# Kernel tuning notes

Hardware: AMD Instinct MI355X
Metric: run time of the kernel (lower is better)

## Reference

```python
import jax, jax.numpy as jnp
import numpy as np

N_DIMS = 64
D1 = N_DIMS - 1          # 63, feature dim of xs and of per-head q/k/v in non-last layers
N_EMBD = 2 * N_DIMS      # 128, forced by H + attn residual
N_LAYER = 12
N_HEAD = 4
POINTS = 512
BS = 16
LN_EPS = 1e-5


def setup_inputs() -> dict:
    key = jax.random.key(0)
    ks = jax.random.split(key, 16)
    s = 0.05
    f32 = jnp.float32
    inp = {
        "xs": jax.random.normal(ks[0], (BS, POINTS, D1), f32),
        "ys": jax.random.normal(ks[1], (BS, POINTS), f32),
        "head_mask": jnp.ones((1, N_HEAD, 1, 1), f32),
        # _read_in
        "read_in_W": jax.random.normal(ks[2], (N_DIMS, N_EMBD), f32) * s,
        "read_in_b": jnp.zeros((N_EMBD,), f32),
        # layers 0..n_layer-2: q/v Linear(D1 -> n_head*D1), key linear is unused (identity repeat)
        "qW": jax.random.normal(ks[3], (N_LAYER - 1, D1, N_HEAD * D1), f32) * s,
        "vW": jax.random.normal(ks[4], (N_LAYER - 1, D1, N_HEAD * D1), f32) * s,
        # last layer: q/k/v Linear(n_embd -> n_head*n_embd)
        "qW_last": jax.random.normal(ks[5], (N_EMBD, N_HEAD * N_EMBD), f32) * s,
        "kW_last": jax.random.normal(ks[6], (N_EMBD, N_HEAD * N_EMBD), f32) * s,
        "vW_last": jax.random.normal(ks[7], (N_EMBD, N_HEAD * N_EMBD), f32) * s,
        # layernorms
        "ln1_g": jnp.ones((N_LAYER, N_EMBD), f32),
        "ln1_b": jnp.zeros((N_LAYER, N_EMBD), f32),
        "ln2_g": jnp.ones((N_LAYER, N_EMBD), f32),
        "ln2_b": jnp.zeros((N_LAYER, N_EMBD), f32),
        # MLPs (n_embd -> 4*n_embd -> n_embd)
        "mlp_W1": jax.random.normal(ks[8], (N_LAYER, N_EMBD, 4 * N_EMBD), f32) * s,
        "mlp_b1": jnp.zeros((N_LAYER, 4 * N_EMBD), f32),
        "mlp_W2": jax.random.normal(ks[9], (N_LAYER, 4 * N_EMBD, N_EMBD), f32) * s,
        "mlp_b2": jnp.zeros((N_LAYER, N_EMBD), f32),
        # _read_out
        "read_out_W": jax.random.normal(ks[10], (N_EMBD, 1), f32) * s,
        "read_out_b": jnp.zeros((1,), f32),
    }
    return inp


def _layernorm(x, g, b):
    mu = jnp.mean(x, axis=-1, keepdims=True)
    var = jnp.var(x, axis=-1, keepdims=True)
    return (x - mu) * jax.lax.rsqrt(var + LN_EPS) * g + b


def _forward(xs, ys, head_mask, read_in_W, read_in_b, qW, vW,
             qW_last, kW_last, vW_last, ln1_g, ln1_b, ln2_g, ln2_b,
             mlp_W1, mlp_b1, mlp_W2, mlp_b2, read_out_W, read_out_b):
    bs, P, d = xs.shape  # d = n_dims - 1
    # _combine: interleave x (zero-padded) and (x, y) rows -> [bs, 2P, n_dims]
    xs_e = jnp.concatenate([xs, jnp.zeros((bs, P, 1), xs.dtype)], axis=2)
    ys_w = jnp.concatenate([xs, ys[:, :, None]], axis=2)
    zs = jnp.stack([xs_e, ys_w], axis=2).reshape(bs, 2 * P, d + 1)
    N = 2 * P

    # triangular count-normalization: row i (0-based) has 1/(i+1) on cols <= i
    i = jnp.arange(N)
    maskNorm = jnp.where(i[None, :] <= i[:, None], 1.0 / (i[:, None] + 1.0), 0.0).astype(xs.dtype)

    H = zs @ read_in_W + read_in_b  # [bs, N, n_embd]

    for idx in range(N_LAYER):
        if idx != N_LAYER - 1:
            # q from the "label half" of H, k is identity on the "feature half", v learned
            q = (H[:, :, N_DIMS:2 * N_DIMS - 1] @ qW[idx]).reshape(bs, N, N_HEAD, D1).transpose(0, 2, 1, 3)
            k = jnp.broadcast_to(H[:, None, :, :D1], (bs, N_HEAD, N, D1))
            v = (H[:, :, :D1] @ vW[idx]).reshape(bs, N, N_HEAD, D1).transpose(0, 2, 1, 3)
            # cat((z1[n_dims zeros], ., z2[1 zero])) -> head dim 2*n_dims == n_embd
            pad = ((0, 0), (0, 0), (0, 0), (N_DIMS, 1))
            q = jnp.pad(q, pad) * head_mask
            k = jnp.pad(k, pad) * head_mask
            v = jnp.pad(v, pad) * head_mask
        else:
            q = (H @ qW_last).reshape(bs, N, N_HEAD, N_EMBD).transpose(0, 2, 1, 3) * head_mask
            k = (H @ kW_last).reshape(bs, N, N_HEAD, N_EMBD).transpose(0, 2, 1, 3) * head_mask
            v = (H @ vW_last).reshape(bs, N, N_HEAD, N_EMBD).transpose(0, 2, 1, 3) * head_mask
        scores = jax.nn.relu(jnp.einsum('bhid,bhjd->bhij', q, k)) * maskNorm  # [bs,h,N,N]
        attn = jnp.einsum('bhij,bhjd->bhid', scores, v).sum(axis=1)           # [bs,N,n_embd]
        H = _layernorm(H + attn, ln1_g[idx], ln1_b[idx])
        mlp = jax.nn.relu(H @ mlp_W1[idx] + mlp_b1[idx]) @ mlp_W2[idx] + mlp_b2[idx]
        H = _layernorm(H + mlp, ln2_g[idx], ln2_b[idx])

    pred = H @ read_out_W + read_out_b  # [bs, N, 1]
    return pred[:, ::2, 0]              # [bs, P]


def reference(xs, ys, head_mask, read_in_W, read_in_b, qW, vW,
              qW_last, kW_last, vW_last, ln1_g, ln1_b, ln2_g, ln2_b,
              mlp_W1, mlp_b1, mlp_W2, mlp_b2, read_out_W, read_out_b):
    return _forward(xs, ys, head_mask, read_in_W, read_in_b, qW, vW,
                    qW_last, kW_last, vW_last, ln1_g, ln1_b, ln2_g, ln2_b,
                    mlp_W1, mlp_b1, mlp_W2, mlp_b2, read_out_W, read_out_b)
```

## Files before the change

### kernel.cpp

```cpp
#include <hip/hip_runtime.h>

#define BS 16
#define SEQ 1024
#define EMB 128
#define NHEAD 4
#define LN_EPS 1e-5f

typedef __attribute__((ext_vector_type(8))) short bf16x8;
typedef __attribute__((ext_vector_type(8))) _Float16 f16x8;
typedef __attribute__((ext_vector_type(4))) float f32x4;
typedef __attribute__((ext_vector_type(4))) unsigned short u16x4;
typedef __attribute__((ext_vector_type(4))) unsigned int u32x4;

__device__ __forceinline__ unsigned short f2b(float f) {
  union { float f; unsigned u; } v; v.f = f;
  unsigned r = v.u + 0x7fff + ((v.u >> 16) & 1);
  return (unsigned short)(r >> 16);
}
__device__ __forceinline__ float b2f(unsigned short u) {
  return __uint_as_float((unsigned)u << 16);
}
__device__ __forceinline__ unsigned short f2h(float f) {
  union { _Float16 h; unsigned short u; } v; v.h = (_Float16)f; return v.u;
}
__device__ __forceinline__ void split2(float x, unsigned short& hi, unsigned short& lo) {
  unsigned short h = f2b(x);
  float hf = __uint_as_float((unsigned)h << 16);
  hi = h; lo = f2b(x - hf);
}
__device__ __forceinline__ float rsqrt_acc(float v) {
  float r = rsqrtf(v);
  return r * (1.5f - 0.5f * v * r * r);
}

__global__ void k_prep_fragT(const float* __restrict__ in, unsigned short* __restrict__ out,
                             size_t PL, int L, int Kin, int Nin, int N, int K) {
  int idx = blockIdx.x * 256 + threadIdx.x;
  int nblk = (N >> 4) * (K >> 5);
  int total = L * N * K;
  if (idx >= total) return;
  int e = idx & 7;
  int lane = (idx >> 3) & 63;
  int blk = (idx >> 9) % nblk;
  int l = idx / (512 * nblk);
  int nb = blk % (N >> 4), kc = blk / (N >> 4);
  int n = nb * 16 + (lane & 15);
  int k = kc * 32 + (lane >> 4) * 8 + e;
  float v = (k < Kin && n < Nin) ? in[(size_t)l * Kin * Nin + (size_t)k * Nin + n] : 0.f;
  unsigned short hi, lo; split2(v, hi, lo);
  out[idx] = hi; out[PL + idx] = lo;
}

__global__ void k_prep_qvfrag(const float* __restrict__ qW, const float* __restrict__ vW,
                              unsigned short* __restrict__ out, size_t PL) {
  int idx = blockIdx.x * 256 + threadIdx.x;
  int total = 11 * 512 * 128;
  if (idx >= total) return;
  int e = idx & 7;
  int lane = (idx >> 3) & 63;
  int blk = (idx >> 9) & 127;
  int l = idx >> 16;
  int nb = blk & 31, kc = blk >> 5;
  int n = nb * 16 + (lane & 15);
  int k = kc * 32 + (lane >> 4) * 8 + e;
  float v = 0.f;
  if (n < 256) {
    int hh = n >> 6, d = n & 63;
    if (d < 63 && k >= 64 && k < 127) v = qW[(size_t)l * 63 * 252 + (size_t)(k - 64) * 252 + hh * 63 + d];
  } else {
    int n2 = n - 256, hh = n2 >> 6, d = n2 & 63;
    if (d < 63 && k < 63) v = vW[(size_t)l * 63 * 252 + (size_t)k * 252 + hh * 63 + d];
  }
  unsigned short hi, lo; split2(v, hi, lo);
  out[idx] = hi; out[PL + idx] = lo;
}

__global__ void k_prep_lastfrag(const float* __restrict__ qW, const float* __restrict__ kW,
                                const float* __restrict__ vW,
                                unsigned short* __restrict__ out, size_t PL) {
  int idx = blockIdx.x * 256 + threadIdx.x;
  int total = 1536 * 128;
  if (idx >= total) return;
  int e = idx & 7;
  int lane = (idx >> 3) & 63;
  int blk = idx >> 9;
  int nb = blk % 96, kc = blk / 96;
  int n = nb * 16 + (lane & 15);
  int k = kc * 32 + (lane >> 4) * 8 + e;
  int tsel = n >> 9, n2 = n & 511;
  const float* W = tsel == 0 ? qW : (tsel == 1 ? kW : vW);
  float v = W[(size_t)k * 512 + n2];
  unsigned short hi, lo; split2(v, hi, lo);
  out[idx] = hi; out[PL + idx] = lo;
}

__global__ void k_combine_readin(const float* __restrict__ xs, const float* __restrict__ ys,
                                 const float* __restrict__ W, const float* __restrict__ bias,
                                 unsigned short* __restrict__ Hbf, size_t hbPl,
                                 unsigned short* __restrict__ Hh) {
  int blk = blockIdx.x;
  int b = blk >> 10, t = blk & 1023, p = t >> 1;
  __shared__ float zs[64];
  int tid = threadIdx.x;
  if (tid < 64) {
    float v;
    if (tid < 63) v = xs[((size_t)b * 512 + p) * 63 + tid];
    else v = (t & 1) ? ys[(size_t)b * 512 + p] : 0.f;
    zs[tid] = v;
  }
  __syncthreads();
  float acc = bias[tid];
  #pragma unroll 8
  for (int d = 0; d < 64; ++d) acc += zs[d] * W[d * 128 + tid];
  size_t o = (size_t)blk * 128 + tid;
  unsigned short hi, lo; split2(acc, hi, lo);
  Hbf[o] = hi; Hbf[hbPl + o] = lo;
  if (tid < 64) Hh[(size_t)blk * 64 + tid] = f2h(acc);
}

template<int MODE, bool RELU>
__global__ __launch_bounds__(256) void k_gemm(
    const unsigned short* __restrict__ A, size_t aPl,
    const unsigned short* __restrict__ BT, size_t bPl, const float* __restrict__ bias,
    int N,
    unsigned short* __restrict__ out0,
    unsigned short* __restrict__ out1,
    unsigned short* __restrict__ out2) {
  extern __shared__ unsigned short lds[];
  int tid = threadIdx.x;
  int wid = tid >> 6, lane = tid & 63;
  int lr = lane & 15, lg = lane >> 4;
  int row0g = blockIdx.x * 64;
  int n0 = blockIdx.y * 64;
  unsigned short* Ah = lds;
  unsigned short* Al = Ah + 64 * 136;
  {
    const unsigned short* gA = A + (size_t)row0g * 128;
    const unsigned short* srcs[2] = { gA, gA + aPl };
    unsigned short* dsts[2] = { Ah, Al };
    #pragma unroll
    for (int p = 0; p < 2; ++p)
      #pragma unroll
      for (int it = 0; it < 4; ++it) {
        int e = it * 2048 + tid * 8;
        bf16x8 v = *reinterpret_cast<const bf16x8*>(srcs[p] + e);
        *reinterpret_cast<bf16x8*>(dsts[p] + (e >> 7) * 136 + (e & 127)) = v;
      }
  }
  __syncthreads();
  bf16x8 afh[4], afl[4];
  #pragma unroll
  for (int kf = 0; kf < 4; ++kf) {
    int o = (wid * 16 + lr) * 136 + kf * 32 + lg * 8;
    afh[kf] = *reinterpret_cast<const bf16x8*>(Ah + o);
    afl[kf] = *reinterpret_cast<const bf16x8*>(Al + o);
  }
  f32x4 acc[4] = {};
  int nhw = N >> 4;
  #pragma unroll
  for (int nf = 0; nf < 4; ++nf) {
    #pragma unroll
    for (int kf = 0; kf < 4; ++kf) {
      size_t bo = ((size_t)kf * nhw + (n0 >> 4) + nf) * 512 + lane * 8;
      bf16x8 bh = *reinterpret_cast<const bf16x8*>(BT + bo);
      bf16x8 bl = *reinterpret_cast<const bf16x8*>(BT + bPl + bo);
      acc[nf] = __builtin_amdgcn_mfma_f32_16x16x32_bf16(afh[kf], bh, acc[nf], 0, 0, 0);
      acc[nf] = __builtin_amdgcn_mfma_f32_16x16x32_bf16(afl[kf], bh, acc[nf], 0, 0, 0);
      acc[nf] = __builtin_amdgcn_mfma_f32_16x16x32_bf16(afh[kf], bl, acc[nf], 0, 0, 0);
    }
  }
  __syncthreads();
  #pragma unroll
  for (int nf = 0; nf < 4; ++nf) {
    int c = n0 + nf * 16 + lr;
    float bv = bias ? bias[c] : 0.f;
    #pragma unroll
    for (int r = 0; r < 4; ++r) {
      float v = acc[nf][r] + bv;
      if (RELU) v = fmaxf(v, 0.f);
      int rL = wid * 16 + lg * 4 + r, cL = nf * 16 + lr;
      ((unsigned short(*)[66])lds)[rL][cL] = f2h(v);
    }
  }
  __syncthreads();
  int u = tid * 2;
  int lane2 = u >> 3, e0 = u & 7;
  if (MODE == 2) {
    unsigned short (*t16)[66] = (unsigned short(*)[66])lds;
    int b = row0g >> 10, t0 = row0g & 1023;
    int tsel = n0 >> 9, c2b = n0 & 511, hh = c2b >> 7, dbase = c2b & 127;
    size_t bh = (size_t)b * NHEAD + hh;
    if (tsel < 2) {
      unsigned short* base = tsel ? out1 : out0;
      int tb0 = t0 >> 4, kc0 = dbase >> 5;
      #pragma unroll
      for (int fb = 0; fb < 8; ++fb) {
        int tbl = fb >> 1, kcl = fb & 1;
        int t_l = tbl * 16 + (lane2 & 15);
        int c_l = kcl * 32 + ((lane2 >> 4) << 3) + e0;
        size_t dst = ((bh * 64 + tb0 + tbl) * 4 + kc0 + kcl) * 512 + lane2 * 8 + e0;
        base[dst] = t16[t_l][c_l];
        base[dst + 1] = t16[t_l][c_l + 1];
      }
    } else {
      int db0 = dbase >> 4, jc0 = t0 >> 5;
      #pragma unroll
      for (int fb = 0; fb < 8; ++fb) {
        int dbl = fb >> 1, jcl = fb & 1;
        int c_l = dbl * 16 + (lane2 & 15);
        int t_l = jcl * 32 + ((lane2 >> 4) << 3) + e0;
        size_t dst = ((bh * 8 + db0 + dbl) * 32 + jc0 + jcl) * 512 + lane2 * 8 + e0;
        out2[dst] = t16[t_l][c_l];
        out2[dst + 1] = t16[t_l + 1][c_l];
      }
    }
  } else {
    unsigned short (*t16)[66] = (unsigned short(*)[66])lds;
    int b = row0g >> 10, t0 = row0g & 1023;
    if (n0 < 256) {
      size_t bh = (size_t)b * NHEAD + (n0 >> 6);
      int tb0 = t0 >> 4;
      #pragma unroll
      for (int fb = 0; fb < 8; ++fb) {
        int tbl = fb >> 1, kcl = fb & 1;
        int t_l = tbl * 16 + (lane2 & 15);
        int c_l = kcl * 32 + ((lane2 >> 4) << 3) + e0;
        size_t dst = ((bh * 64 + tb0 + tbl) * 2 + kcl) * 512 + lane2 * 8 + e0;
        out0[dst] = t16[t_l][c_l];
        out0[dst + 1] = t16[t_l][c_l + 1];
      }
    } else {
      size_t bh = (size_t)b * NHEAD + ((n0 - 256) >> 6);
      int jc0 = t0 >> 5;
      #pragma unroll
      for (int fb = 0; fb < 8; ++fb) {
        int dbl = fb >> 1, jcl = fb & 1;
        int c_l = dbl * 16 + (lane2 & 15);
        int t_l = jcl * 32 + ((lane2 >> 4) << 3) + e0;
        size_t dst = ((bh * 4 + dbl) * 32 + jc0 + jcl) * 512 + lane2 * 8 + e0;
        out1[dst] = t16[t_l][c_l];
        out1[dst + 1] = t16[t_l + 1][c_l];
      }
    }
  }
}

__global__ __launch_bounds__(512) void k_attn_v7(
    const unsigned short* __restrict__ q,
    const unsigned short* __restrict__ Hh,
    const unsigned short* __restrict__ vT,
    const float* __restrict__ head_mask,
    const unsigned short* __restrict__ HbfIn, unsigned short* __restrict__ HbfOut, size_t hbPl,
    const float* __restrict__ g, const float* __restrict__ bta) {
  extern __shared__ char sh[];
  int bid = blockIdx.x;
  int xcd = bid & 7, u = bid >> 3;
  int b = xcd * 2 + (u >> 4);
  int pidx = u & 15;
  int tid = threadIdx.x;
  int wid = tid >> 6, lane = tid & 63;
  int h = wid & 3, grp = wid >> 2;
  int lr = lane & 15, lg = lane >> 4;
  int i0t[2] = { pidx * 32, (31 - pidx) * 32 };
  int NSS = (33 - pidx) >> 1;

  const char* gK = (const char*)(Hh + (size_t)b * SEQ * 64);
  char* KB = sh;
  unsigned short* sw = (unsigned short*)(sh + 16384 + wid * 2560);

  const unsigned short* qh = q + (size_t)(b * NHEAD + h) * 65536;
  const unsigned short* vh = vT + (size_t)(b * NHEAD + h) * 65536;

  f16x8 qf[2][2][2];
  #pragma unroll
  for (int t = 0; t < 2; ++t)
    #pragma unroll
    for (int mf = 0; mf < 2; ++mf)
      #pragma unroll
      for (int kf = 0; kf < 2; ++kf)
        qf[t][mf][kf] = *reinterpret_cast<const f16x8*>(
            qh + ((((i0t[t] >> 4) + mf) * 2 + kf) << 9) + lane * 8);
  f32x4 oacc[2][2][4] = {};

  u32x4 sreg;
  auto SLOAD = [&](int ss) {
    sreg = *reinterpret_cast<const u32x4*>(gK + (size_t)ss * 8192 + tid * 16);
  };
  auto SWRITE = [&](int buf) {
    int row = tid >> 3, colb = (tid & 7) * 16;
    *reinterpret_cast<u32x4*>(KB + buf * 8192 + row * 128 + (colb ^ ((row & 7) << 4))) = sreg;
  };

  SLOAD(0); SWRITE(0);
  __syncthreads();

  for (int ss = 0; ss < NSS; ++ss) {
    int cur = ss & 1;
    bool more = (ss + 1 < NSS);
    if (more) SLOAD(ss + 1);
    int js = ss * 64 + grp * 32;
    if (js < i0t[1] + 32) {
      f16x8 vch[4];
      #pragma unroll
      for (int nf = 0; nf < 4; ++nf)
        vch[nf] = *reinterpret_cast<const f16x8*>(vh + ((nf * 32 + (js >> 5)) << 9) + lane * 8);
      f16x8 kfr[2][2];
      #pragma unroll
      for (int nf2 = 0; nf2 < 2; ++nf2)
        #pragma unroll
        for (int kf = 0; kf < 2; ++kf) {
          int row = grp * 32 + nf2 * 16 + lr;
          int colb = kf * 64 + lg * 16;
          kfr[nf2][kf] = *reinterpret_cast<const f16x8*>(
              KB + cur * 8192 + row * 128 + (colb ^ ((row & 7) << 4)));
        }
      #pragma unroll
      for (int t = 0; t < 2; ++t) {
        if (js < i0t[t] + 32) {
          #pragma unroll
          for (int nf2 = 0; nf2 < 2; ++nf2) {
            #pragma unroll
            for (int mf = 0; mf < 2; ++mf) {
              f32x4 sacc = {};
              #pragma unroll
              for (int kf = 0; kf < 2; ++kf)
                sacc = __builtin_amdgcn_mfma_f32_16x16x32_f16(qf[t][mf][kf], kfr[nf2][kf], sacc, 0, 0, 0);
              #pragma unroll
              for (int r = 0; r < 4; ++r) {
                int i = i0t[t] + mf * 16 + lg * 4 + r;
                int j = js + nf2 * 16 + lr;
                float v = (j <= i) ? fmaxf(sacc[r], 0.f) : 0.f;
                sw[(mf * 16 + lg * 4 + r) * 40 + nf2 * 16 + lr] = f2h(v);
              }
            }
          }
          asm volatile("s_waitcnt lgkmcnt(0)" ::: "memory");
          __builtin_amdgcn_sched_barrier(0);
          #pragma unroll
          for (int mf = 0; mf < 2; ++mf) {
            f16x8 sf = *reinterpret_cast<const f16x8*>(&sw[(mf * 16 + lr) * 40 + lg * 8]);
            #pragma unroll
            for (int nf = 0; nf < 4; ++nf)
              oacc[t][mf][nf] = __builtin_amdgcn_mfma_f32_16x16x32_f16(sf, vch[nf], oacc[t][mf][nf], 0, 0, 0);
          }
        }
      }
    }
    if (more) SWRITE(cur ^ 1);
    __syncthreads();
  }

  float hm = head_mask[h];
  float hm3 = hm * hm * hm;
  float* f8 = (float*)sh;
  for (int t = 0; t < 2; ++t) {
    #pragma unroll
    for (int mf = 0; mf < 2; ++mf)
      #pragma unroll
      for (int nf = 0; nf < 4; ++nf)
        #pragma unroll
        for (int r = 0; r < 4; ++r)
          f8[wid * 2048 + (mf * 16 + lg * 4 + r) * 64 + nf * 16 + lr] = oacc[t][mf][nf][r] * hm3;
    __syncthreads();
    for (int idx = tid; idx < 8192; idx += 512) f8[idx] += f8[idx + 8192];
    __syncthreads();
    for (int idx = tid; idx < 4096; idx += 512) f8[idx] += f8[idx + 4096];
    __syncthreads();
    for (int idx = tid; idx < 2048; idx += 512) {
      int rr = idx >> 6;
      f8[idx] = (f8[idx] + f8[idx + 2048]) / (float)(i0t[t] + rr + 1);
    }
    __syncthreads();
    for (int rl = 0; rl < 4; ++rl) {
      int rr = wid * 4 + rl;
      size_t row = ((size_t)b * SEQ + i0t[t] + rr) * EMB;
      int c0 = lane, c1 = lane + 64;
      float x0 = b2f(HbfIn[row + c0]) + b2f(HbfIn[hbPl + row + c0]);
      float x1 = b2f(HbfIn[row + c1]) + b2f(HbfIn[hbPl + row + c1]) + f8[rr * 64 + lane];
      float s1 = x0 + x1, s2 = x0 * x0 + x1 * x1;
      #pragma unroll
      for (int off = 1; off < 64; off <<= 1) {
        s1 += __shfl_xor(s1, off);
        s2 += __shfl_xor(s2, off);
      }
      float mu = s1 * (1.f / 128.f);
      float var = s2 * (1.f / 128.f) - mu * mu;
      float rs = rsqrt_acc(var + LN_EPS);
      float y0 = (x0 - mu) * rs * g[c0] + bta[c0];
      float y1 = (x1 - mu) * rs * g[c1] + bta[c1];
      unsigned short h0, l0, h1, l1; split2(y0, h0, l0); split2(y1, h1, l1);
      HbfOut[row + c0] = h0; HbfOut[hbPl + row + c0] = l0;
      HbfOut[row + c1] = h1; HbfOut[hbPl + row + c1] = l1;
    }
    __syncthreads();
  }
}

__global__ __launch_bounds__(512) void k_attn_fused(
    const unsigned short* __restrict__ q,
    const unsigned short* __restrict__ kbuf,
    const unsigned short* __restrict__ vT,
    const float* __restrict__ head_mask,
    const unsigned short* __restrict__ HbfIn, unsigned short* __restrict__ HbfOut, size_t hbPl,
    const float* __restrict__ g, const float* __restrict__ bta) {
  constexpr int KF = 4, NFO = 8;
  constexpr int NT = SEQ / 32;
  extern __shared__ char sh[];
  int bid = blockIdx.x;
  int xcd = bid & 7, u = bid >> 3;
  int b = xcd * 2 + (u >> 4);
  int pidx = u & 15;
  int tid = threadIdx.x;
  int wid = tid >> 6, lane = tid & 63;
  int h = wid & 3, grp = wid >> 2;
  int lr = lane & 15, lg = lane >> 4;
  unsigned short* sw = (unsigned short*)(sh + wid * 2560);
  const unsigned short* qh = q + (size_t)(b * NHEAD + h) * 131072;
  const unsigned short* kh = kbuf + (size_t)(b * NHEAD + h) * 131072;
  const unsigned short* vh = vT + (size_t)(b * NHEAD + h) * 131072;
  float hm = head_mask[h];
  float hm3 = hm * hm * hm;

  for (int s = 0; s < 2; ++s) {
    int tile = (s == 0) ? pidx : (NT - 1 - pidx);
    int i0 = tile * 32;
    f16x8 qf[2][KF];
    #pragma unroll
    for (int mf = 0; mf < 2; ++mf)
      #pragma unroll
      for (int kf = 0; kf < KF; ++kf)
        qf[mf][kf] = *reinterpret_cast<const f16x8*>(
            qh + ((((i0 >> 4) + mf) * 4 + kf) << 9) + lane * 8);
    f32x4 oacc[2][NFO] = {};
    int jend = i0 + 32;
    for (int j0 = grp * 32; j0 < jend; j0 += 64) {
      f16x8 vch[NFO];
      #pragma unroll
      for (int nf = 0; nf < NFO; ++nf)
        vch[nf] = *reinterpret_cast<const f16x8*>(vh + ((nf * 32 + (j0 >> 5)) << 9) + lane * 8);
      #pragma unroll
      for (int nf2 = 0; nf2 < 2; ++nf2) {
        f16x8 kfr[KF];
        #pragma unroll
        for (int kf = 0; kf < KF; ++kf)
          kfr[kf] = *reinterpret_cast<const f16x8*>(
              kh + ((((j0 >> 4) + nf2) * 4 + kf) << 9) + lane * 8);
        #pragma unroll
        for (int mf = 0; mf < 2; ++mf) {
          f32x4 sacc = {};
          #pragma unroll
          for (int kf = 0; kf < KF; ++kf)
            sacc = __builtin_amdgcn_mfma_f32_16x16x32_f16(qf[mf][kf], kfr[kf], sacc, 0, 0, 0);
          #pragma unroll
          for (int r = 0; r < 4; ++r) {
            int i = i0 + mf * 16 + lg * 4 + r;
            int j = j0 + nf2 * 16 + lr;
            float v = (j <= i) ? fmaxf(sacc[r], 0.f) : 0.f;
            sw[(mf * 16 + lg * 4 + r) * 40 + nf2 * 16 + lr] = f2h(v);
          }
        }
      }
      asm volatile("s_waitcnt lgkmcnt(0)" ::: "memory");
      __builtin_amdgcn_sched_barrier(0);
      #pragma unroll
      for (int mf = 0; mf < 2; ++mf) {
        f16x8 sf = *reinterpret_cast<const f16x8*>(&sw[(mf * 16 + lr) * 40 + lg * 8]);
        #pragma unroll
        for (int nf = 0; nf < NFO; ++nf)
          oacc[mf][nf] = __builtin_amdgcn_mfma_f32_16x16x32_f16(sf, vch[nf], oacc[mf][nf], 0, 0, 0);
      }
    }
    float* f8 = (float*)sh;
    __syncthreads();
    if (wid < 4) {
      #pragma unroll
      for (int mf = 0; mf < 2; ++mf)
        #pragma unroll
        for (int nf = 0; nf < NFO; ++nf)
          #pragma unroll
          for (int r = 0; r < 4; ++r)
            f8[(wid & 3) * 4096 + (mf * 16 + lg * 4 + r) * 128 + nf * 16 + lr] = oacc[mf][nf][r] * hm3;
    }
    __syncthreads();
    if (wid >= 4) {
      #pragma unroll
      for (int mf = 0; mf < 2; ++mf)
        #pragma unroll
        for (int nf = 0; nf < NFO; ++nf)
          #pragma unroll
          for (int r = 0; r < 4; ++r)
            f8[(wid & 3) * 4096 + (mf * 16 + lg * 4 + r) * 128 + nf * 16 + lr] += oacc[mf][nf][r] * hm3;
    }
    __syncthreads();
    for (int idx = tid; idx < 8192; idx += 512) f8[idx] += f8[idx + 8192];
    __syncthreads();
    for (int idx = tid; idx < 4096; idx += 512) {
      int rr = idx >> 7;
      f8[idx] = (f8[idx] + f8[idx + 4096]) / (float)(i0 + rr + 1);
    }
    __syncthreads();
    for (int rl = 0; rl < 4; ++rl) {
      int rr = wid * 4 + rl;
      size_t row = ((size_t)b * SEQ + i0 + rr) * EMB;
      int c0 = lane, c1 = lane + 64;
      float x0 = b2f(HbfIn[row + c0]) + b2f(HbfIn[hbPl + row + c0]) + f8[rr * 128 + c0];
      float x1 = b2f(HbfIn[row + c1]) + b2f(HbfIn[hbPl + row + c1]) + f8[rr * 128 + c1];
      float s1 = x0 + x1, s2 = x0 * x0 + x1 * x1;
      #pragma unroll
      for (int off = 1; off < 64; off <<= 1) {
        s1 += __shfl_xor(s1, off);
        s2 += __shfl_xor(s2, off);
      }
      float mu = s1 * (1.f / 128.f);
      float var = s2 * (1.f / 128.f) - mu * mu;
      float rs = rsqrt_acc(var + LN_EPS);
      float y0 = (x0 - mu) * rs * g[c0] + bta[c0];
      float y1 = (x1 - mu) * rs * g[c1] + bta[c1];
      unsigned short h0, l0, h1, l1; split2(y0, h0, l0); split2(y1, h1, l1);
      HbfOut[row + c0] = h0; HbfOut[hbPl + row + c0] = l0;
      HbfOut[row + c1] = h1; HbfOut[hbPl + row + c1] = l1;
    }
    __syncthreads();
  }
}

template<bool LAST>
__global__ __launch_bounds__(256) void k_mlpf(
    const unsigned short* __restrict__ A, size_t aPl,
    const unsigned short* __restrict__ W1, size_t w1Pl, const float* __restrict__ b1,
    const unsigned short* __restrict__ W2, size_t w2Pl, const float* __restrict__ b2,
    unsigned short* __restrict__ HbfOut, size_t hbPl,
    unsigned short* __restrict__ Hh, float* __restrict__ Hst,
    const float* __restrict__ g, const float* __restrict__ bta) {
  extern __shared__ unsigned short mlds[];
  unsigned short* As = mlds;
  unsigned short* Mid = mlds + 4096;
  float* yb = (float*)Mid;
  int tid = threadIdx.x;
  int wid = tid >> 6, lane = tid & 63;
  int lr = lane & 15, lg = lane >> 4;
  int row0g = blockIdx.x * 16;
  {
    const unsigned short* gA = A + (size_t)row0g * 128;
    int row = tid >> 4;
    int sc = ((tid & 15) * 8) ^ ((row & 7) << 3);
    *reinterpret_cast<bf16x8*>(As + row * 128 + sc) =
        *reinterpret_cast<const bf16x8*>(gA + tid * 8);
    *reinterpret_cast<bf16x8*>(As + 2048 + row * 128 + sc) =
        *reinterpret_cast<const bf16x8*>(gA + aPl + tid * 8);
  }
  __syncthreads();
  bf16x8 afh[4], afl[4];
  #pragma unroll
  for (int kf = 0; kf < 4; ++kf) {
    int o = lr * 128 + ((kf * 32 + lg * 8) ^ ((lr & 7) << 3));
    afh[kf] = *reinterpret_cast<const bf16x8*>(As + o);
    afl[kf] = *reinterpret_cast<const bf16x8*>(As + 2048 + o);
  }
  bf16x8 cwh[4], cwl[4], nwh[4], nwl[4];
  #pragma unroll
  for (int kf = 0; kf < 4; ++kf) {
    size_t bo = ((size_t)kf * 32 + wid * 8) * 512 + lane * 8;
    cwh[kf] = *reinterpret_cast<const bf16x8*>(W1 + bo);
    cwl[kf] = *reinterpret_cast<const bf16x8*>(W1 + w1Pl + bo);
  }
  #pragma unroll
  for (int j = 0; j < 8; ++j) {
    int ntile = wid * 8 + j;
    if (j < 7) {
      #pragma unroll
      for (int kf = 0; kf < 4; ++kf) {
        size_t bo = ((size_t)kf * 32 + ntile + 1) * 512 + lane * 8;
        nwh[kf] = *reinterpret_cast<const bf16x8*>(W1 + bo);
        nwl[kf] = *reinterpret_cast<const bf16x8*>(W1 + w1Pl + bo);
      }
    }
    f32x4 acc = {};
    #pragma unroll
    for (int kf = 0; kf < 4; ++kf) {
      acc = __builtin_amdgcn_mfma_f32_16x16x32_bf16(afh[kf], cwh[kf], acc, 0, 0, 0);
      acc = __builtin_amdgcn_mfma_f32_16x16x32_bf16(afl[kf], cwh[kf], acc, 0, 0, 0);
      acc = __builtin_amdgcn_mfma_f32_16x16x32_bf16(afh[kf], cwl[kf], acc, 0, 0, 0);
    }
    int c = ntile * 16 + lr;
    float bv = b1[c];
    int kc = c >> 5, sub = ((c & 31) >> 3) * 128 + (c & 7);
    #pragma unroll
    for (int r = 0; r < 4; ++r) {
      float v = fmaxf(acc[r] + bv, 0.f);
      unsigned short hi, lo; split2(v, hi, lo);
      int ma = kc * 512 + sub + (lg * 4 + r) * 8;
      Mid[ma] = hi;
      Mid[8192 + ma] = lo;
    }
    if (j < 7) {
      #pragma unroll
      for (int kf = 0; kf < 4; ++kf) { cwh[kf] = nwh[kf]; cwl[kf] = nwl[kf]; }
    }
  }
  __syncthreads();
  f32x4 acc2[2] = {};
  bf16x8 c2h[2], c2l[2], n2h[2], n2l[2];
  #pragma unroll
  for (int j = 0; j < 2; ++j) {
    size_t bo = (size_t)(wid * 2 + j) * 512 + lane * 8;
    c2h[j] = *reinterpret_cast<const bf16x8*>(W2 + bo);
    c2l[j] = *reinterpret_cast<const bf16x8*>(W2 + w2Pl + bo);
  }
  #pragma unroll
  for (int kc = 0; kc < 16; ++kc) {
    if (kc < 15) {
      #pragma unroll
      for (int j = 0; j < 2; ++j) {
        size_t bo = ((size_t)(kc + 1) * 8 + wid * 2 + j) * 512 + lane * 8;
        n2h[j] = *reinterpret_cast<const bf16x8*>(W2 + bo);
        n2l[j] = *reinterpret_cast<const bf16x8*>(W2 + w2Pl + bo);
      }
    }
    int o = kc * 512 + lane * 8;
    bf16x8 amh = *reinterpret_cast<const bf16x8*>(Mid + o);
    bf16x8 aml = *reinterpret_cast<const bf16x8*>(Mid + 8192 + o);
    #pragma unroll
    for (int j = 0; j < 2; ++j) {
      acc2[j] = __builtin_amdgcn_mfma_f32_16x16x32_bf16(amh, c2h[j], acc2[j], 0, 0, 0);
      acc2[j] = __builtin_amdgcn_mfma_f32_16x16x32_bf16(aml, c2h[j], acc2[j], 0, 0, 0);
      acc2[j] = __builtin_amdgcn_mfma_f32_16x16x32_bf16(amh, c2l[j], acc2[j], 0, 0, 0);
    }
    if (kc < 15) {
      c2h[0] = n2h[0]; c2h[1] = n2h[1];
      c2l[0] = n2l[0]; c2l[1] = n2l[1];
    }
  }
  __syncthreads();
  #pragma unroll
  for (int j = 0; j < 2; ++j) {
    int c = (wid * 2 + j) * 16 + lr;
    float bv = b2[c];
    #pragma unroll
    for (int r = 0; r < 4; ++r) {
      int row = lg * 4 + r;
      int sc = c ^ ((row & 7) << 3);
      float yres = b2f(As[row * 128 + sc]) + b2f(As[2048 + row * 128 + sc]);
      yb[row * 132 + c] = acc2[j][r] + bv + yres;
    }
  }
  __syncthreads();
  for (int rl = 0; rl < 4; ++rl) {
    int row = wid * 4 + rl;
    size_t gro = (size_t)(row0g + row) * EMB;
    int c0 = lane, c1 = lane + 64;
    float x0 = yb[row * 132 + c0];
    float x1 = yb[row * 132 + c1];
    float s1 = x0 + x1, s2 = x0 * x0 + x1 * x1;
    #pragma unroll
    for (int off = 1; off < 64; off <<= 1) {
      s1 += __shfl_xor(s1, off);
      s2 += __shfl_xor(s2, off);
    }
    float mu = s1 * (1.f / 128.f);
    float var = s2 * (1.f / 128.f) - mu * mu;
    float rs = rsqrt_acc(var + LN_EPS);
    float y0 = (x0 - mu) * rs * g[c0] + bta[c0];
    float y1 = (x1 - mu) * rs * g[c1] + bta[c1];
    unsigned short h0, l0, h1, l1; split2(y0, h0, l0); split2(y1, h1, l1);
    HbfOut[gro + c0] = h0; HbfOut[hbPl + gro + c0] = l0;
    HbfOut[gro + c1] = h1; HbfOut[hbPl + gro + c1] = l1;
    Hh[(size_t)(row0g + row) * 64 + lane] = f2h(y0);
    if (LAST) { Hst[gro + c0] = y0; Hst[gro + c1] = y1; }
  }
}

__global__ __launch_bounds__(64) void k_readout(const float* __restrict__ H,
                                                const float* __restrict__ W, const float* __restrict__ b0,
                                                float* __restrict__ out) {
  int idx = blockIdx.x;
  int b = idx >> 9, p = idx & 511;
  size_t row = ((size_t)b * SEQ + 2 * p) * EMB;
  int lane = threadIdx.x;
  float acc = H[row + lane] * W[lane] + H[row + 64 + lane] * W[64 + lane];
  #pragma unroll
  for (int off = 1; off < 64; off <<= 1) acc += __shfl_xor(acc, off);
  if (lane == 0) out[idx] = acc + b0[0];
}

extern "C" void kernel_launch(void* const* d_in, const int* in_sizes, int n_in,
                              void* d_out, int out_size, void* d_ws, size_t ws_size,
                              hipStream_t stream) {
  (void)in_sizes; (void)n_in; (void)out_size; (void)ws_size;
  const float* xs        = (const float*)d_in[0];
  const float* ys        = (const float*)d_in[1];
  const float* head_mask = (const float*)d_in[2];
  const float* read_in_W = (const float*)d_in[3];
  const float* read_in_b = (const float*)d_in[4];
  const float* qW        = (const float*)d_in[5];
  const float* vW        = (const float*)d_in[6];
  const float* qW_last   = (const float*)d_in[7];
  const float* kW_last   = (const float*)d_in[8];
  const float* vW_last   = (const float*)d_in[9];
  const float* ln1_g     = (const float*)d_in[10];
  const float* ln1_b     = (const float*)d_in[11];
  const float* ln2_g     = (const float*)d_in[12];
  const float* ln2_b     = (const float*)d_in[13];
  const float* mlp_W1    = (const float*)d_in[14];
  const float* mlp_b1    = (const float*)d_in[15];
  const float* mlp_W2    = (const float*)d_in[16];
  const float* mlp_b2    = (const float*)d_in[17];
  const float* ro_W      = (const float*)d_in[18];
  const float* ro_b      = (const float*)d_in[19];

  const size_t HPL   = (size_t)BS * SEQ * EMB;
  const size_t QVWPL = (size_t)11 * 512 * 128;
  const size_t W1PL  = (size_t)12 * 512 * 128;
  const size_t W2PL  = (size_t)12 * 512 * 128;
  const size_t LASTPL= (size_t)1536 * 128;
  const size_t VOFF  = (size_t)BS * NHEAD * 65536;

  char* ws = (char*)d_ws;
  size_t off = 0;
  auto alloc = [&](size_t bytes) -> void* {
    void* p = ws + off;
    off += (bytes + 255) & ~(size_t)255;
    return p;
  };
  float* H             = (float*)alloc(HPL * 4);
  unsigned short* Hbf  = (unsigned short*)alloc(2 * HPL * 2);
  unsigned short* Hbf2 = (unsigned short*)alloc(2 * HPL * 2);
  unsigned short* Hh   = (unsigned short*)alloc((size_t)BS * SEQ * 64 * 2);
  unsigned short* qbuf = (unsigned short*)alloc((size_t)BS * NHEAD * 131072 * 2);
  unsigned short* kmid = (unsigned short*)alloc((size_t)BS * NHEAD * 131072 * 2);
  unsigned short* vTl  = (unsigned short*)alloc((size_t)BS * NHEAD * 131072 * 2);
  unsigned short* qvWT = (unsigned short*)alloc(2 * QVWPL * 2);
  unsigned short* W1T  = (unsigned short*)alloc(2 * W1PL * 2);
  unsigned short* W2T  = (unsigned short*)alloc(2 * W2PL * 2);
  unsigned short* lastT= (unsigned short*)alloc(2 * LASTPL * 2);

  { int tot = 11 * 512 * 128; k_prep_qvfrag<<<dim3((tot + 255) / 256), 256, 0, stream>>>(qW, vW, qvWT, QVWPL); }
  { int tot = 12 * 512 * 128; k_prep_fragT<<<dim3((tot + 255) / 256), 256, 0, stream>>>(mlp_W1, W1T, W1PL, 12, 128, 512, 512, 128); }
  { int tot = 12 * 512 * 128; k_prep_fragT<<<dim3((tot + 255) / 256), 256, 0, stream>>>(mlp_W2, W2T, W2PL, 12, 512, 128, 128, 512); }
  { int tot = 1536 * 128; k_prep_lastfrag<<<dim3((tot + 255) / 256), 256, 0, stream>>>(qW_last, kW_last, vW_last, lastT, LASTPL); }

  k_combine_readin<<<dim3(BS * SEQ), 128, 0, stream>>>(xs, ys, read_in_W, read_in_b, Hbf, HPL, Hh);

  const int GEMM_LDS = 2 * 64 * 136 * 2;
  const int MLPF_LDS = (4096 + 16384) * 2;

  for (int l = 0; l < 11; ++l) {
    k_gemm<3, false><<<dim3(256, 8), 256, GEMM_LDS, stream>>>(
        Hbf, HPL, qvWT + (size_t)l * 65536, QVWPL, nullptr, 512,
        qbuf, qbuf + VOFF, nullptr);
    k_attn_v7<<<dim3(256), 512, 65536, stream>>>(
        qbuf, Hh, qbuf + VOFF, head_mask, Hbf, Hbf2, HPL, ln1_g + l * 128, ln1_b + l * 128);
    k_mlpf<false><<<dim3(1024), 256, MLPF_LDS, stream>>>(
        Hbf2, HPL, W1T + (size_t)l * 65536, W1PL, mlp_b1 + l * 512,
        W2T + (size_t)l * 65536, W2PL, mlp_b2 + l * 128,
        Hbf, HPL, Hh, nullptr, ln2_g + l * 128, ln2_b + l * 128);
  }
  k_gemm<2, false><<<dim3(256, 24), 256, GEMM_LDS, stream>>>(
      Hbf, HPL, lastT, LASTPL, nullptr, 1536, qbuf, kmid, vTl);
  k_attn_fused<<<dim3(256), 512, 65536, stream>>>(
      qbuf, kmid, vTl, head_mask, Hbf, Hbf2, HPL, ln1_g + 11 * 128, ln1_b + 11 * 128);
  k_mlpf<true><<<dim3(1024), 256, MLPF_LDS, stream>>>(
      Hbf2, HPL, W1T + (size_t)11 * 65536, W1PL, mlp_b1 + 11 * 512,
      W2T + (size_t)11 * 65536, W2PL, mlp_b2 + 11 * 128,
      Hbf, HPL, Hh, H, ln2_g + 11 * 128, ln2_b + 11 * 128);

  k_readout<<<dim3(8192), 64, 0, stream>>>(H, ro_W, ro_b, (float*)d_out);
}
```

Before: 925.4 us.

## Fuse next layer's q/v projection GEMM into MLP epilogue kernel

The MLP kernel for layers 0-9 now computes the next layer's q/v projection from its freshly normalized 16-row tile using MFMA with split bf16 hi/lo operands. It stages the results in LDS and scatters them into the fragment layouts that the attention kernel expects. Only the first layer's q/v GEMM remains a standalone launch, which removes ten kernel launches and a reread of H from global memory. In exchange the MLP kernel gains extra register pressure, LDS use and scattered 16-bit global stores, and each block streams the full 128x512 weight slice.

```diff
diff --git a/kernel.cpp b/kernel.cpp
--- a/kernel.cpp
+++ b/kernel.cpp
@@ -524,18 +524,21 @@
   }
 }
 
-template<bool LAST>
+template<int MM>
 __global__ __launch_bounds__(256) void k_mlpf(
     const unsigned short* __restrict__ A, size_t aPl,
     const unsigned short* __restrict__ W1, size_t w1Pl, const float* __restrict__ b1,
     const unsigned short* __restrict__ W2, size_t w2Pl, const float* __restrict__ b2,
     unsigned short* __restrict__ HbfOut, size_t hbPl,
     unsigned short* __restrict__ Hh, float* __restrict__ Hst,
-    const float* __restrict__ g, const float* __restrict__ bta) {
+    const float* __restrict__ g, const float* __restrict__ bta,
+    const unsigned short* __restrict__ QW, size_t qwPl,
+    unsigned short* __restrict__ qOut, unsigned short* __restrict__ vOut) {
   extern __shared__ unsigned short mlds[];
   unsigned short* As = mlds;
   unsigned short* Mid = mlds + 4096;
   float* yb = (float*)Mid;
+  unsigned short* st = Mid + 8192;
   int tid = threadIdx.x;
   int wid = tid >> 6, lane = tid & 63;
   int lr = lane & 15, lg = lane >> 4;
@@ -666,7 +669,89 @@
     HbfOut[gro + c0] = h0; HbfOut[hbPl + gro + c0] = l0;
     HbfOut[gro + c1] = h1; HbfOut[hbPl + gro + c1] = l1;
     Hh[(size_t)(row0g + row) * 64 + lane] = f2h(y0);
-    if (LAST) { Hst[gro + c0] = y0; Hst[gro + c1] = y1; }
+    if (MM == 2) { Hst[gro + c0] = y0; Hst[gro + c1] = y1; }
+    if (MM == 0) { yb[row * 132 + c0] = y0; yb[row * 132 + c1] = y1; }
+  }
+  if (MM != 0) return;
+  __syncthreads();
+  bf16x8 yfh[4], yfl[4];
+  #pragma unroll
+  for (int kf = 0; kf < 4; ++kf)
+    #pragma unroll
+    for (int e = 0; e < 8; ++e) {
+      float v = yb[lr * 132 + kf * 32 + lg * 8 + e];
+      unsigned short hi, lo; split2(v, hi, lo);
+      yfh[kf][e] = (short)hi; yfl[kf][e] = (short)lo;
+    }
+  bf16x8 qwh[4], qwl[4], xwh[4], xwl[4];
+  #pragma unroll
+  for (int kf = 0; kf < 4; ++kf) {
+    size_t bo = ((size_t)kf * 32 + wid * 8) * 512 + lane * 8;
+    qwh[kf] = *reinterpret_cast<const bf16x8*>(QW + bo);
+    qwl[kf] = *reinterpret_cast<const bf16x8*>(QW + qwPl + bo);
+  }
+  #pragma unroll
+  for (int j = 0; j < 8; ++j) {
+    int ntile = wid * 8 + j;
+    if (j < 7) {
+      #pragma unroll
+      for (int kf = 0; kf < 4; ++kf) {
+        size_t bo = ((size_t)kf * 32 + ntile + 1) * 512 + lane * 8;
+        xwh[kf] = *reinterpret_cast<const bf16x8*>(QW + bo);
+        xwl[kf] = *reinterpret_cast<const bf16x8*>(QW + qwPl + bo);
+      }
+    }
+    f32x4 acc = {};
+    #pragma unroll
+    for (int kf = 0; kf < 4; ++kf) {
+      acc = __builtin_amdgcn_mfma_f32_16x16x32_bf16(yfh[kf], qwh[kf], acc, 0, 0, 0);
+      acc = __builtin_amdgcn_mfma_f32_16x16x32_bf16(yfl[kf], qwh[kf], acc, 0, 0, 0);
+      acc = __builtin_amdgcn_mfma_f32_16x16x32_bf16(yfh[kf], qwl[kf], acc, 0, 0, 0);
+    }
+    int c = ntile * 16 + lr;
+    #pragma unroll
+    for (int r = 0; r < 4; ++r)
+      st[(lg * 4 + r) * 512 + c] = f2h(acc[r]);
+    if (j < 7) {
+      #pragma unroll
+      for (int kf = 0; kf < 4; ++kf) { qwh[kf] = xwh[kf]; qwl[kf] = xwl[kf]; }
+    }
+  }
+  __syncthreads();
+  int b = row0g >> 10, t0 = row0g & 1023;
+  int tb = t0 >> 4, jc = t0 >> 5, tbpar = tb & 1;
+  {
+    int u2 = tid * 2;
+    int lane2 = u2 >> 3, e0 = u2 & 7;
+    #pragma unroll
+    for (int fb = 0; fb < 8; ++fb) {
+      int hh = fb >> 1, kcl = fb & 1;
+      size_t bh = (size_t)b * NHEAD + hh;
+      int t_l = lane2 & 15;
+      int c_l = hh * 64 + kcl * 32 + ((lane2 >> 4) << 3) + e0;
+      size_t dst = ((bh * 64 + tb) * 2 + kcl) * 512 + lane2 * 8 + e0;
+      qOut[dst] = st[t_l * 512 + c_l];
+      qOut[dst + 1] = st[t_l * 512 + c_l + 1];
+    }
+  }
+  {
+    int sel = tid >> 7;
+    int idx2 = tid & 127;
+    int wl = idx2 * 2;
+    int ll = wl >> 3, ev = wl & 7;
+    int t_l = ((ll >> 4) << 3) + ev;
+    int d_l = ll & 15;
+    #pragma unroll
+    for (int p = 0; p < 8; ++p) {
+      int vb = p * 2 + sel;
+      int hh = vb >> 2, db = vb & 3;
+      size_t bh = (size_t)b * NHEAD + hh;
+      int n = 256 + hh * 64 + db * 16 + d_l;
+      unsigned int pack = (unsigned)st[t_l * 512 + n] |
+                          ((unsigned)st[(t_l + 1) * 512 + n] << 16);
+      size_t dstu16 = ((bh * 4 + db) * 32 + jc) * 512 + tbpar * 256 + wl;
+      *reinterpret_cast<unsigned int*>(vOut + dstu16) = pack;
+    }
   }
 }
 
@@ -744,25 +829,34 @@
   const int GEMM_LDS = 2 * 64 * 136 * 2;
   const int MLPF_LDS = (4096 + 16384) * 2;
 
+  k_gemm<3, false><<<dim3(256, 8), 256, GEMM_LDS, stream>>>(
+      Hbf, HPL, qvWT, QVWPL, nullptr, 512, qbuf, qbuf + VOFF, nullptr);
+
   for (int l = 0; l < 11; ++l) {
-    k_gemm<3, false><<<dim3(256, 8), 256, GEMM_LDS, stream>>>(
-        Hbf, HPL, qvWT + (size_t)l * 65536, QVWPL, nullptr, 512,
-        qbuf, qbuf + VOFF, nullptr);
     k_attn_v7<<<dim3(256), 512, 65536, stream>>>(
         qbuf, Hh, qbuf + VOFF, head_mask, Hbf, Hbf2, HPL, ln1_g + l * 128, ln1_b + l * 128);
-    k_mlpf<false><<<dim3(1024), 256, MLPF_LDS, stream>>>(
-        Hbf2, HPL, W1T + (size_t)l * 65536, W1PL, mlp_b1 + l * 512,
-        W2T + (size_t)l * 65536, W2PL, mlp_b2 + l * 128,
-        Hbf, HPL, Hh, nullptr, ln2_g + l * 128, ln2_b + l * 128);
+    if (l < 10)
+      k_mlpf<0><<<dim3(1024), 256, MLPF_LDS, stream>>>(
+          Hbf2, HPL, W1T + (size_t)l * 65536, W1PL, mlp_b1 + l * 512,
+          W2T + (size_t)l * 65536, W2PL, mlp_b2 + l * 128,
+          Hbf, HPL, Hh, nullptr, ln2_g + l * 128, ln2_b + l * 128,
+          qvWT + (size_t)(l + 1) * 65536, QVWPL, qbuf, qbuf + VOFF);
+    else
+      k_mlpf<1><<<dim3(1024), 256, MLPF_LDS, stream>>>(
+          Hbf2, HPL, W1T + (size_t)l * 65536, W1PL, mlp_b1 + l * 512,
+          W2T + (size_t)l * 65536, W2PL, mlp_b2 + l * 128,
+          Hbf, HPL, Hh, nullptr, ln2_g + l * 128, ln2_b + l * 128,
+          nullptr, 0, nullptr, nullptr);
   }
   k_gemm<2, false><<<dim3(256, 24), 256, GEMM_LDS, stream>>>(
       Hbf, HPL, lastT, LASTPL, nullptr, 1536, qbuf, kmid, vTl);
   k_attn_fused<<<dim3(256), 512, 65536, stream>>>(
       qbuf, kmid, vTl, head_mask, Hbf, Hbf2, HPL, ln1_g + 11 * 128, ln1_b + 11 * 128);
-  k_mlpf<true><<<dim3(1024), 256, MLPF_LDS, stream>>>(
+  k_mlpf<2><<<dim3(1024), 256, MLPF_LDS, stream>>>(
       Hbf2, HPL, W1T + (size_t)11 * 65536, W1PL, mlp_b1 + 11 * 512,
       W2T + (size_t)11 * 65536, W2PL, mlp_b2 + 11 * 128,
-      Hbf, HPL, Hh, H, ln2_g + 11 * 128, ln2_b + 11 * 128);
+      Hbf, HPL, Hh, H, ln2_g + 11 * 128, ln2_b + 11 * 128,
+      nullptr, 0, nullptr, nullptr);
 
   k_readout<<<dim3(8192), 64, 0, stream>>>(H, ro_W, ro_b, (float*)d_out);
 }
```

Measured after the change: 1.075 ms. 1.16x slower.
